# Kernel tuning notes

Hardware: AMD Instinct MI355X
Metric: run time of the kernel (lower is better)

## Reference

```python
import jax, jax.numpy as jnp
import numpy as np

N_NODES = 50000
N_EDGES = 800000
N_GRAPHS = 2500
HIDDEN = 64
IN_DIM = 14  # 11 QM9 features + 3 pos


def setup_inputs() -> dict:
    key = jax.random.key(0)
    ks = jax.random.split(key, 12)
    def glorot(k, shape):
        fan_in = shape[0]
        return jax.random.normal(k, shape, dtype=jnp.float32) / np.sqrt(fan_in)
    return {
        "x": jax.random.normal(ks[0], (N_NODES, 11), dtype=jnp.float32),
        "pos": jax.random.normal(ks[1], (N_NODES, 3), dtype=jnp.float32),
        "edge_index": jax.random.randint(ks[2], (2, N_EDGES), 0, N_NODES, dtype=jnp.int64),
        "batch": jnp.sort(jax.random.randint(ks[3], (N_NODES,), 0, N_GRAPHS, dtype=jnp.int64)),
        "W1a": glorot(ks[4], (IN_DIM, HIDDEN)),
        "b1a": jnp.zeros((HIDDEN,), jnp.float32),
        "W1b": glorot(ks[5], (HIDDEN, HIDDEN)),
        "b1b": jnp.zeros((HIDDEN,), jnp.float32),
        "W2a": glorot(ks[6], (HIDDEN, HIDDEN)),
        "b2a": jnp.zeros((HIDDEN,), jnp.float32),
        "W2b": glorot(ks[7], (HIDDEN, HIDDEN)),
        "b2b": jnp.zeros((HIDDEN,), jnp.float32),
        "Wlin": glorot(ks[8], (HIDDEN, 1)),
        "blin": jnp.zeros((1,), jnp.float32),
    }


def reference(x, pos, edge_index, batch, W1a, b1a, W1b, b1b, W2a, b2a, W2b, b2b, Wlin, blin):
    n = x.shape[0]
    src, dst = edge_index[0], edge_index[1]

    def gin_conv(h, Wa, ba, Wb, bb):
        # GINConv (eps=0): nn((1+eps)*h + sum_{j in N(i)} h_j)
        agg = jax.ops.segment_sum(h[src], dst, num_segments=n)  # scatter-add over edges
        z = h + agg
        return jax.nn.relu(z @ Wa + ba) @ Wb + bb

    h = jnp.concatenate([x, pos], axis=1)  # [N, 14]
    h = jax.nn.relu(gin_conv(h, W1a, b1a, W1b, b1b))
    h = jax.nn.relu(gin_conv(h, W2a, b2a, W2b, b2b))

    # global_mean_pool over graph ids
    sums = jax.ops.segment_sum(h, batch, num_segments=N_GRAPHS)            # [G, H]
    counts = jax.ops.segment_sum(jnp.ones((n,), h.dtype), batch, num_segments=N_GRAPHS)
    pooled = sums / jnp.maximum(counts, 1.0)[:, None]
    return pooled @ Wlin + blin  # [G, 1]
```

## Files before the change

### kernel.cpp

```cpp
#include <hip/hip_runtime.h>
#include <hip/hip_fp16.h>


typedef unsigned int uint;
typedef _Float16 half8 __attribute__((ext_vector_type(8)));
typedef float f32x4 __attribute__((ext_vector_type(4)));

#define BSH   6
#define NBKMAX 1024
#define EPB   4096
#define CAPSH 11
#define CAP   (1 << CAPSH)
#define ZBLK  64

__device__ __forceinline__ void addu(float* a, uint d) {
    __half2 h = *(__half2*)&d;
    a[0] += __low2float(h);
    a[1] += __high2float(h);
}
__device__ __forceinline__ half8 as_half8(uint4 u) {
    union { uint4 u; half8 h; } x; x.u = u; return x.h;
}


__global__ __launch_bounds__(256) void pack_bin(
    const float* __restrict__ x, const float* __restrict__ pos,
    uint2* __restrict__ xp2,
    const int* __restrict__ src, const int* __restrict__ dst,
    int* __restrict__ bkt_cnt, uint* __restrict__ pairs,
    const float* __restrict__ W1a, const float* __restrict__ W1b,
    const float* __restrict__ W2a, const float* __restrict__ W2b,
    _Float16* __restrict__ wp1a, _Float16* __restrict__ wp1b,
    _Float16* __restrict__ wp2a, _Float16* __restrict__ wp2b,
    uint4* __restrict__ zbuf, int nz4,
    int packb, int nbk, int N, int E)
{
    int bx = (int)blockIdx.x;
    if (bx < ZBLK) {
        uint4 z4 = {0u, 0u, 0u, 0u};
        for (int idx = bx * 256 + threadIdx.x; idx < nz4; idx += ZBLK * 256)
            zbuf[idx] = z4;
        return;
    }
    bx -= ZBLK;
    if (bx == 0) {
        for (int idx = threadIdx.x; idx < 64 * 32; idx += 256) {
            int n = idx >> 5, k = idx & 31;
            wp1a[idx] = (k < 14) ? (_Float16)W1a[k * 64 + n] : (_Float16)0.f;
        }
        for (int idx = threadIdx.x; idx < 64 * 64; idx += 256) {
            int n = idx >> 6, k = idx & 63;
            wp1b[idx] = (_Float16)W1b[k * 64 + n];
            wp2a[idx] = (_Float16)W2a[k * 64 + n];
            wp2b[idx] = (_Float16)W2b[k * 64 + n];
        }
        return;
    }
    bx -= 1;
    if (bx < packb) {
        int i = bx * 256 + threadIdx.x;
        if (i >= N) return;
        float v[16];
#pragma unroll
        for (int k = 0; k < 11; k++) v[k] = x[(size_t)i * 11 + k];
        v[11] = pos[(size_t)i * 3 + 0];
        v[12] = pos[(size_t)i * 3 + 1];
        v[13] = pos[(size_t)i * 3 + 2];
        v[14] = 0.f; v[15] = 0.f;
#pragma unroll
        for (int c = 0; c < 4; c++) {
            __half2 l = __floats2half2_rn(v[4 * c],     v[4 * c + 1]);
            __half2 h = __floats2half2_rn(v[4 * c + 2], v[4 * c + 3]);
            uint2 u;
            u.x = *(uint*)&l;
            u.y = *(uint*)&h;
            xp2[(size_t)i * 4 + c] = u;
        }
        return;
    }
    bx -= packb;
    __shared__ int lcnt[NBKMAX];
    __shared__ int lbase[NBKMAX];
    for (int i = threadIdx.x; i < nbk; i += 256) lcnt[i] = 0;
    __syncthreads();
    int e0 = bx * EPB + threadIdx.x;
    uint pv[EPB / 256];
    int  rk[EPB / 256], bk[EPB / 256];
#pragma unroll
    for (int j = 0; j < EPB / 256; j++) {
        int e = e0 + j * 256;
        bk[j] = -1;
        if (e < E) {
            int s = src[e];
            int d = dst[e];
            bk[j] = d >> BSH;
            pv[j] = ((uint)(d & ((1 << BSH) - 1)) << 16) | (uint)s;
            rk[j] = atomicAdd(&lcnt[bk[j]], 1);
        }
    }
    __syncthreads();
    for (int i = threadIdx.x; i < nbk; i += 256) {
        int c = lcnt[i];
        lbase[i] = c ? atomicAdd(&bkt_cnt[i], c) : 0;
    }
    __syncthreads();
#pragma unroll
    for (int j = 0; j < EPB / 256; j++) {
        if (bk[j] >= 0) {
            int p = lbase[bk[j]] + rk[j];
            if (p < CAP)
                pairs[((size_t)bk[j] << CAPSH) + p] = pv[j];
        }
    }
}


__global__ __launch_bounds__(256) void bucket_build(
    const uint* __restrict__ pairs, const int* __restrict__ bkt_cnt,
    int* __restrict__ offs, int* __restrict__ deg,
    int* __restrict__ ssrc, int N)
{
    __shared__ int cnt[256];
    __shared__ int cur[256];
    __shared__ int wsum[4];
    int b = blockIdx.x;
    int nbase = b << BSH;
    int nn = min(1 << BSH, N - nbase);
    cnt[threadIdx.x] = 0;
    __syncthreads();
    int start = b << CAPSH;
    int end = start + min(bkt_cnt[b], CAP);
    for (int e = start + threadIdx.x; e < end; e += 256)
        atomicAdd(&cnt[pairs[e] >> 16], 1);
    __syncthreads();
    int v = cnt[threadIdx.x];
    int lane = threadIdx.x & 63, w = threadIdx.x >> 6;
    int s = v;
#pragma unroll
    for (int off2 = 1; off2 < 64; off2 <<= 1) {
        int t = __shfl_up(s, off2, 64);
        if (lane >= off2) s += t;
    }
    if (lane == 63) wsum[w] = s;
    __syncthreads();
    int add = 0;
    for (int j = 0; j < w; j++) add += wsum[j];
    int gofs = start + (s + add - v);
    if (threadIdx.x < nn) {
        offs[nbase + threadIdx.x] = gofs;
        deg[nbase + threadIdx.x]  = v;
    }
    cur[threadIdx.x] = gofs;
    __syncthreads();
    for (int e = start + threadIdx.x; e < end; e += 256) {
        uint pr = pairs[e];
        int p = atomicAdd(&cur[pr >> 16], 1);
        ssrc[p] = (int)(pr & 0xffffu);
    }
}


__global__ __launch_bounds__(256) void gather1_mlp1(
    const uint2* __restrict__ xp2,
    const int* __restrict__ offs, const int* __restrict__ deg,
    const int* __restrict__ ssrc,
    const _Float16* __restrict__ wp1a, const _Float16* __restrict__ wp1b,
    const float* __restrict__ b1a, const float* __restrict__ b1b,
    uint* __restrict__ h1p)
{
    __shared__ uint4 zb[16 * 2];
    __shared__ float hb[16 * 68];
    int lane = threadIdx.x & 63;
    int wid  = threadIdx.x >> 6;
    int i0 = blockIdx.x << 4;
    int n0 = i0 + wid * 4;

    int stv = 0, lnv = 0;
    if (lane < 4) { stv = offs[n0 + lane]; lnv = deg[n0 + lane]; }
    int j4 = lane >> 2, c = lane & 3;
    int svp[4];
#pragma unroll
    for (int t = 0; t < 4; t++) {
        int st = __shfl(stv, t, 64), len = __shfl(lnv, t, 64);
        if (len > 0) svp[t] = ssrc[st + min(lane, len - 1)];
    }
    for (int t = 0; t < 4; t++) {
        int i = n0 + t;
        int st = __shfl(stv, t, 64), len = __shfl(lnv, t, 64);
        uint2 S = xp2[(size_t)i * 4 + c];
        float a[4] = {0.f, 0.f, 0.f, 0.f};
        int k = 0;
        while (k < len) {
            int chunk = min(len - k, 64);
            int sv = (k == 0) ? svp[t]
                              : ssrc[st + k + min(lane, chunk - 1)];
            int tt = 0;
            for (; tt + 32 <= chunk; tt += 32) {
                int sA = __shfl(sv, tt + j4, 64);
                int sB = __shfl(sv, tt + 16 + j4, 64);
                uint2 A = xp2[(size_t)sA * 4 + c];
                uint2 B = xp2[(size_t)sB * 4 + c];
                addu(a + 0, A.x); addu(a + 2, A.y);
                addu(a + 0, B.x); addu(a + 2, B.y);
            }
            for (; tt + 16 <= chunk; tt += 16) {
                int sA = __shfl(sv, tt + j4, 64);
                uint2 A = xp2[(size_t)sA * 4 + c];
                addu(a + 0, A.x); addu(a + 2, A.y);
            }
            if (tt < chunk) {
                int r = chunk - tt;
                int sA = __shfl(sv, tt + min(j4, r - 1), 64);
                uint2 A = xp2[(size_t)sA * 4 + c];
                if (j4 < r) { addu(a + 0, A.x); addu(a + 2, A.y); }
            }
            k += chunk;
        }
#pragma unroll
        for (int mm = 4; mm < 64; mm <<= 1)
#pragma unroll
            for (int d = 0; d < 4; d++) a[d] += __shfl_xor(a[d], mm, 64);
        addu(a + 0, S.x); addu(a + 2, S.y);
        if (lane < 4) {
            __half2 l  = __floats2half2_rn(a[0], a[1]);
            __half2 hh = __floats2half2_rn(a[2], a[3]);
            uint2 u;
            u.x = *(uint*)&l;
            u.y = *(uint*)&hh;
            ((uint2*)zb)[(wid * 4 + t) * 4 + lane] = u;
        }
    }
    __syncthreads();

    int m = lane & 15, quad = lane >> 4;
    int half = lane >> 5, p = lane & 31;
    int nw = wid * 16 + m;
    half8 BA  = *(const half8*)(wp1a + (size_t)nw * 32 + quad * 8);
    half8 BB0 = *(const half8*)(wp1b + (size_t)nw * 64 + quad * 8);
    half8 BB1 = *(const half8*)(wp1b + (size_t)nw * 64 + 32 + quad * 8);
    float baw = b1a[nw], bbw = b1b[nw];

    half8 A0;
#pragma unroll
    for (int jj = 0; jj < 8; jj++) A0[jj] = (_Float16)0.f;
    if (quad < 2)
        A0 = as_half8(zb[m * 2 + quad]);
    f32x4 acc = (f32x4){baw, baw, baw, baw};
    acc = __builtin_amdgcn_mfma_f32_16x16x32_f16(A0, BA, acc, 0, 0, 0);
#pragma unroll
    for (int r = 0; r < 4; r++)
        hb[(quad * 4 + r) * 68 + wid * 16 + m] = fmaxf(acc[r], 0.f);
    __syncthreads();
    half8 A1[2];
#pragma unroll
    for (int hh = 0; hh < 2; hh++)
#pragma unroll
        for (int jj = 0; jj < 8; jj++)
            A1[hh][jj] = (_Float16)hb[m * 68 + hh * 32 + quad * 8 + jj];
    f32x4 acc2 = (f32x4){bbw, bbw, bbw, bbw};
    acc2 = __builtin_amdgcn_mfma_f32_16x16x32_f16(A1[0], BB0, acc2, 0, 0, 0);
    acc2 = __builtin_amdgcn_mfma_f32_16x16x32_f16(A1[1], BB1, acc2, 0, 0, 0);
    __syncthreads();
#pragma unroll
    for (int r = 0; r < 4; r++)
        hb[(quad * 4 + r) * 68 + wid * 16 + m] = fmaxf(acc2[r], 0.f);
    __syncthreads();
#pragma unroll
    for (int it = 0; it < 2; it++) {
        int row = wid * 4 + it * 2 + half;
        float lo = hb[row * 68 + 2 * p];
        float hi = hb[row * 68 + 2 * p + 1];
        __half2 hh2 = __floats2half2_rn(lo, hi);
        h1p[(size_t)(i0 + row) * 32 + p] = *(uint*)&hh2;
    }
}


__global__ __launch_bounds__(256) void gather2_mlp2pool(
    const uint4* __restrict__ h4,
    const int* __restrict__ offs, const int* __restrict__ deg,
    const int* __restrict__ ssrc,
    const _Float16* __restrict__ wp2a, const _Float16* __restrict__ wp2b,
    const float* __restrict__ b2a, const float* __restrict__ b2b,
    const int* __restrict__ batch,
    float* __restrict__ sums, float* __restrict__ counts)
{
    __shared__ uint4 zb[16 * 8];
    __shared__ float hb[16 * 68];
    int lane = threadIdx.x & 63;
    int wid  = threadIdx.x >> 6;
    int i0 = blockIdx.x << 4;
    int n0 = i0 + wid * 4;

    int stv = 0, lnv = 0;
    if (lane < 4) { stv = offs[n0 + lane]; lnv = deg[n0 + lane]; }
    int j8 = lane >> 3, q = lane & 7;
    int svp[4];
#pragma unroll
    for (int t = 0; t < 4; t++) {
        int st = __shfl(stv, t, 64), len = __shfl(lnv, t, 64);
        if (len > 0) svp[t] = ssrc[st + min(lane, len - 1)];
    }
    for (int t = 0; t < 4; t++) {
        int i = n0 + t;
        int st = __shfl(stv, t, 64), len = __shfl(lnv, t, 64);
        uint4 S = h4[(size_t)i * 8 + q];
        float a[8] = {0.f, 0.f, 0.f, 0.f, 0.f, 0.f, 0.f, 0.f};
        int k = 0;
        while (k < len) {
            int chunk = min(len - k, 64);
            int sv = (k == 0) ? svp[t]
                              : ssrc[st + k + min(lane, chunk - 1)];
            int tt = 0;
            for (; tt + 32 <= chunk; tt += 32) {
                int sA = __shfl(sv, tt + j8, 64);
                int sB = __shfl(sv, tt + 8 + j8, 64);
                int sC = __shfl(sv, tt + 16 + j8, 64);
                int sD = __shfl(sv, tt + 24 + j8, 64);
                uint4 A = h4[(size_t)sA * 8 + q];
                uint4 B = h4[(size_t)sB * 8 + q];
                uint4 C = h4[(size_t)sC * 8 + q];
                uint4 D = h4[(size_t)sD * 8 + q];
                addu(a + 0, A.x); addu(a + 2, A.y); addu(a + 4, A.z); addu(a + 6, A.w);
                addu(a + 0, B.x); addu(a + 2, B.y); addu(a + 4, B.z); addu(a + 6, B.w);
                addu(a + 0, C.x); addu(a + 2, C.y); addu(a + 4, C.z); addu(a + 6, C.w);
                addu(a + 0, D.x); addu(a + 2, D.y); addu(a + 4, D.z); addu(a + 6, D.w);
            }
            for (; tt + 16 <= chunk; tt += 16) {
                int sA = __shfl(sv, tt + j8, 64);
                int sB = __shfl(sv, tt + 8 + j8, 64);
                uint4 A = h4[(size_t)sA * 8 + q];
                uint4 B = h4[(size_t)sB * 8 + q];
                addu(a + 0, A.x); addu(a + 2, A.y); addu(a + 4, A.z); addu(a + 6, A.w);
                addu(a + 0, B.x); addu(a + 2, B.y); addu(a + 4, B.z); addu(a + 6, B.w);
            }
            for (; tt + 8 <= chunk; tt += 8) {
                int sA = __shfl(sv, tt + j8, 64);
                uint4 A = h4[(size_t)sA * 8 + q];
                addu(a + 0, A.x); addu(a + 2, A.y); addu(a + 4, A.z); addu(a + 6, A.w);
            }
            if (tt < chunk) {
                int r = chunk - tt;
                int sA = __shfl(sv, tt + min(j8, r - 1), 64);
                uint4 A = h4[(size_t)sA * 8 + q];
                if (j8 < r) {
                    addu(a + 0, A.x); addu(a + 2, A.y);
                    addu(a + 4, A.z); addu(a + 6, A.w);
                }
            }
            k += chunk;
        }
#pragma unroll
        for (int mm = 8; mm < 64; mm <<= 1)
#pragma unroll
            for (int d = 0; d < 8; d++) a[d] += __shfl_xor(a[d], mm, 64);
        addu(a + 0, S.x); addu(a + 2, S.y); addu(a + 4, S.z); addu(a + 6, S.w);
        if (lane < 8) {
            __half2 p0 = __floats2half2_rn(a[0], a[1]);
            __half2 p1 = __floats2half2_rn(a[2], a[3]);
            __half2 p2 = __floats2half2_rn(a[4], a[5]);
            __half2 p3 = __floats2half2_rn(a[6], a[7]);
            uint4 o4;
            o4.x = *(uint*)&p0; o4.y = *(uint*)&p1;
            o4.z = *(uint*)&p2; o4.w = *(uint*)&p3;
            zb[(wid * 4 + t) * 8 + lane] = o4;
        }
    }
    __syncthreads();

    int m = lane & 15, quad = lane >> 4;
    int nw = wid * 16 + m;
    half8 BA0 = *(const half8*)(wp2a + (size_t)nw * 64 + quad * 8);
    half8 BA1 = *(const half8*)(wp2a + (size_t)nw * 64 + 32 + quad * 8);
    half8 BB0 = *(const half8*)(wp2b + (size_t)nw * 64 + quad * 8);
    half8 BB1 = *(const half8*)(wp2b + (size_t)nw * 64 + 32 + quad * 8);
    float baw = b2a[nw], bbw = b2b[nw];

    half8 A0[2];
#pragma unroll
    for (int hh = 0; hh < 2; hh++)
        A0[hh] = as_half8(zb[m * 8 + hh * 4 + quad]);
    f32x4 acc = (f32x4){baw, baw, baw, baw};
    acc = __builtin_amdgcn_mfma_f32_16x16x32_f16(A0[0], BA0, acc, 0, 0, 0);
    acc = __builtin_amdgcn_mfma_f32_16x16x32_f16(A0[1], BA1, acc, 0, 0, 0);
#pragma unroll
    for (int r = 0; r < 4; r++)
        hb[(quad * 4 + r) * 68 + wid * 16 + m] = fmaxf(acc[r], 0.f);
    __syncthreads();
    half8 A1[2];
#pragma unroll
    for (int hh = 0; hh < 2; hh++)
#pragma unroll
        for (int jj = 0; jj < 8; jj++)
            A1[hh][jj] = (_Float16)hb[m * 68 + hh * 32 + quad * 8 + jj];
    f32x4 acc2 = (f32x4){bbw, bbw, bbw, bbw};
    acc2 = __builtin_amdgcn_mfma_f32_16x16x32_f16(A1[0], BB0, acc2, 0, 0, 0);
    acc2 = __builtin_amdgcn_mfma_f32_16x16x32_f16(A1[1], BB1, acc2, 0, 0, 0);
    __syncthreads();
#pragma unroll
    for (int r = 0; r < 4; r++)
        hb[(quad * 4 + r) * 68 + wid * 16 + m] = fmaxf(acc2[r], 0.f);
    __syncthreads();

    int gcur = batch[i0 + wid * 4]; float ps = 0.f; int cntn = 0;
#pragma unroll
    for (int nn = 0; nn < 4; nn++) {
        int row = wid * 4 + nn;
        float v = hb[row * 68 + lane];
        int gi = batch[i0 + row];
        if (gi != gcur) {
            atomicAdd(&sums[gcur * 64 + lane], ps);
            if (lane == 0) atomicAdd(&counts[gcur], (float)cntn);
            gcur = gi; ps = 0.f; cntn = 0;
        }
        ps += v; cntn++;
    }
    atomicAdd(&sums[gcur * 64 + lane], ps);
    if (lane == 0) atomicAdd(&counts[gcur], (float)cntn);
}

__global__ __launch_bounds__(256) void gin_final(
    const float* __restrict__ sums, const float* __restrict__ counts,
    const float* __restrict__ Wlin, const float* __restrict__ blin,
    float* __restrict__ out, int G)
{
    int lane = threadIdx.x & 63;
    int g    = blockIdx.x * 4 + (threadIdx.x >> 6);
    if (g < G) {
        float v = sums[g * 64 + lane] * Wlin[lane];
#pragma unroll
        for (int off = 32; off > 0; off >>= 1) v += __shfl_down(v, off, 64);
        if (lane == 0) out[g] = v / fmaxf(counts[g], 1.0f) + blin[0];
    }
}

extern "C" void kernel_launch(void* const* d_in, const int* in_sizes, int n_in,
                              void* d_out, int out_size, void* d_ws, size_t ws_size,
                              hipStream_t stream) {
    const float* x    = (const float*)d_in[0];
    const float* pos  = (const float*)d_in[1];
    const int*   ei   = (const int*)d_in[2];
    const int*   batch= (const int*)d_in[3];
    const float* W1a  = (const float*)d_in[4];
    const float* b1a  = (const float*)d_in[5];
    const float* W1b  = (const float*)d_in[6];
    const float* b1b  = (const float*)d_in[7];
    const float* W2a  = (const float*)d_in[8];
    const float* b2a  = (const float*)d_in[9];
    const float* W2b  = (const float*)d_in[10];
    const float* b2b  = (const float*)d_in[11];
    const float* Wlin = (const float*)d_in[12];
    const float* blin = (const float*)d_in[13];
    float* out = (float*)d_out;

    const int N = in_sizes[0] / 11;
    const int E = in_sizes[2] / 2;
    const int G = out_size;

    const int* src = ei;
    const int* dst = ei + E;
    const int nbk   = (N + (1 << BSH) - 1) >> BSH;
    const int packb = (N + 255) / 256;
    const int neb   = (E + EPB - 1) / EPB;
    const int NG    = N >> 4;

    char* ws = (char*)d_ws;
    size_t o = 0;
    float* sums    = (float*)(ws + o); o += (size_t)G * 64 * 4;
    float* counts  = (float*)(ws + o); o += (((size_t)G + 63) & ~(size_t)63) * 4;
    const int nz4  = (int)(((size_t)G * 64 + (((size_t)G + 63) & ~(size_t)63)) / 4);
    int*   bkt_cnt = (int*)(ws + o);   o += NBKMAX * 4;
    o = (o + 255) & ~(size_t)255;
    _Float16* wp1a = (_Float16*)(ws + o); o += 64 * 32 * 2;
    o = (o + 255) & ~(size_t)255;
    _Float16* wp1b = (_Float16*)(ws + o); o += 64 * 64 * 2;
    o = (o + 255) & ~(size_t)255;
    _Float16* wp2a = (_Float16*)(ws + o); o += 64 * 64 * 2;
    o = (o + 255) & ~(size_t)255;
    _Float16* wp2b = (_Float16*)(ws + o); o += 64 * 64 * 2;
    o = (o + 255) & ~(size_t)255;
    int*   offs    = (int*)(ws + o);   o += (size_t)N * 4;
    int*   deg     = (int*)(ws + o);   o += (size_t)N * 4;
    o = (o + 255) & ~(size_t)255;
    int*   ssrc    = (int*)(ws + o);   o += ((size_t)nbk << CAPSH) * 4;
    o = (o + 255) & ~(size_t)255;
    uint*  h1p     = (uint*)(ws + o);  o += (size_t)N * 32 * 4;
    o = (o + 255) & ~(size_t)255;
    uint2* xp2     = (uint2*)(ws + o); o += (size_t)N * 32;
    o = (o + 255) & ~(size_t)255;
    uint*  pairs   = (uint*)(ws + o);  o += ((size_t)nbk << CAPSH) * 4;

    hipMemsetAsync(bkt_cnt, 0, NBKMAX * 4, stream);

    pack_bin<<<ZBLK + 1 + packb + neb, 256, 0, stream>>>(
        x, pos, xp2, src, dst, bkt_cnt, pairs,
        W1a, W1b, W2a, W2b, wp1a, wp1b, wp2a, wp2b,
        (uint4*)sums, nz4, packb, nbk, N, E);
    bucket_build<<<nbk, 256, 0, stream>>>(pairs, bkt_cnt, offs, deg, ssrc, N);
    gather1_mlp1<<<NG, 256, 0, stream>>>(
        xp2, offs, deg, ssrc, wp1a, wp1b, b1a, b1b, h1p);
    gather2_mlp2pool<<<NG, 256, 0, stream>>>(
        (const uint4*)h1p, offs, deg, ssrc, wp2a, wp2b, b2a, b2b,
        batch, sums, counts);
    gin_final<<<(G + 3) / 4, 256, 0, stream>>>(
        sums, counts, Wlin, blin, out, G);
}
```

Baseline: 160.9 us.

## Replace bucketed CSR build with direct atomic scatter into fixed-capacity neighbor slots

Drops the two-pass bucket binning plus the bucket_build kernel. Each edge now takes a slot with a global atomicAdd on its destination's degree and writes its source into a padded per-node neighbor array of 64 entries. The gather kernels then read a node's neighbors from a fixed offset, with no offsets array and no chunk loop. This removes one kernel launch and an intermediate pass over the edges. In exchange it adds 800k global atomics, scattered 4-byte writes into a 12.8MB array, and silently drops any edges beyond 64 per node. Neighbor order is also no longer deterministic.

Result: slower. 195.9 us (+21.8%).

```diff
diff --git a/kernel.cpp b/kernel.cpp
--- a/kernel.cpp
+++ b/kernel.cpp
@@ -6,12 +6,9 @@
 typedef _Float16 half8 __attribute__((ext_vector_type(8)));
 typedef float f32x4 __attribute__((ext_vector_type(4)));
 
-#define BSH   6
-#define NBKMAX 1024
-#define EPB   4096
-#define CAPSH 11
-#define CAP   (1 << CAPSH)
-#define ZBLK  64
+#define EPB   1024
+#define ZBLK  32
+#define CAPN  64
 
 __device__ __forceinline__ void addu(float* a, uint d) {
     __half2 h = *(__half2*)&d;
@@ -23,17 +20,17 @@
 }
 
 
-__global__ __launch_bounds__(256) void pack_bin(
+__global__ __launch_bounds__(256) void pack_scatter(
     const float* __restrict__ x, const float* __restrict__ pos,
     uint2* __restrict__ xp2,
     const int* __restrict__ src, const int* __restrict__ dst,
-    int* __restrict__ bkt_cnt, uint* __restrict__ pairs,
+    int* __restrict__ deg, int* __restrict__ nbr,
     const float* __restrict__ W1a, const float* __restrict__ W1b,
     const float* __restrict__ W2a, const float* __restrict__ W2b,
     _Float16* __restrict__ wp1a, _Float16* __restrict__ wp1b,
     _Float16* __restrict__ wp2a, _Float16* __restrict__ wp2b,
     uint4* __restrict__ zbuf, int nz4,
-    int packb, int nbk, int N, int E)
+    int packb, int N, int E)
 {
     int bx = (int)blockIdx.x;
     if (bx < ZBLK) {
@@ -79,91 +76,24 @@
         return;
     }
     bx -= packb;
-    __shared__ int lcnt[NBKMAX];
-    __shared__ int lbase[NBKMAX];
-    for (int i = threadIdx.x; i < nbk; i += 256) lcnt[i] = 0;
-    __syncthreads();
     int e0 = bx * EPB + threadIdx.x;
-    uint pv[EPB / 256];
-    int  rk[EPB / 256], bk[EPB / 256];
 #pragma unroll
     for (int j = 0; j < EPB / 256; j++) {
         int e = e0 + j * 256;
-        bk[j] = -1;
         if (e < E) {
             int s = src[e];
             int d = dst[e];
-            bk[j] = d >> BSH;
-            pv[j] = ((uint)(d & ((1 << BSH) - 1)) << 16) | (uint)s;
-            rk[j] = atomicAdd(&lcnt[bk[j]], 1);
-        }
-    }
-    __syncthreads();
-    for (int i = threadIdx.x; i < nbk; i += 256) {
-        int c = lcnt[i];
-        lbase[i] = c ? atomicAdd(&bkt_cnt[i], c) : 0;
-    }
-    __syncthreads();
-#pragma unroll
-    for (int j = 0; j < EPB / 256; j++) {
-        if (bk[j] >= 0) {
-            int p = lbase[bk[j]] + rk[j];
-            if (p < CAP)
-                pairs[((size_t)bk[j] << CAPSH) + p] = pv[j];
-        }
-    }
-}
-
-
-__global__ __launch_bounds__(256) void bucket_build(
-    const uint* __restrict__ pairs, const int* __restrict__ bkt_cnt,
-    int* __restrict__ offs, int* __restrict__ deg,
-    int* __restrict__ ssrc, int N)
-{
-    __shared__ int cnt[256];
-    __shared__ int cur[256];
-    __shared__ int wsum[4];
-    int b = blockIdx.x;
-    int nbase = b << BSH;
-    int nn = min(1 << BSH, N - nbase);
-    cnt[threadIdx.x] = 0;
-    __syncthreads();
-    int start = b << CAPSH;
-    int end = start + min(bkt_cnt[b], CAP);
-    for (int e = start + threadIdx.x; e < end; e += 256)
-        atomicAdd(&cnt[pairs[e] >> 16], 1);
-    __syncthreads();
-    int v = cnt[threadIdx.x];
-    int lane = threadIdx.x & 63, w = threadIdx.x >> 6;
-    int s = v;
-#pragma unroll
-    for (int off2 = 1; off2 < 64; off2 <<= 1) {
-        int t = __shfl_up(s, off2, 64);
-        if (lane >= off2) s += t;
-    }
-    if (lane == 63) wsum[w] = s;
-    __syncthreads();
-    int add = 0;
-    for (int j = 0; j < w; j++) add += wsum[j];
-    int gofs = start + (s + add - v);
-    if (threadIdx.x < nn) {
-        offs[nbase + threadIdx.x] = gofs;
-        deg[nbase + threadIdx.x]  = v;
-    }
-    cur[threadIdx.x] = gofs;
-    __syncthreads();
-    for (int e = start + threadIdx.x; e < end; e += 256) {
-        uint pr = pairs[e];
-        int p = atomicAdd(&cur[pr >> 16], 1);
-        ssrc[p] = (int)(pr & 0xffffu);
+            int r = atomicAdd(&deg[d], 1);
+            if (r < CAPN)
+                nbr[((size_t)d << 6) + r] = s;
+        }
     }
 }
 
 
 __global__ __launch_bounds__(256) void gather1_mlp1(
     const uint2* __restrict__ xp2,
-    const int* __restrict__ offs, const int* __restrict__ deg,
-    const int* __restrict__ ssrc,
+    const int* __restrict__ deg, const int* __restrict__ nbr,
     const _Float16* __restrict__ wp1a, const _Float16* __restrict__ wp1b,
     const float* __restrict__ b1a, const float* __restrict__ b1b,
     uint* __restrict__ h1p)
@@ -175,46 +105,40 @@
     int i0 = blockIdx.x << 4;
     int n0 = i0 + wid * 4;
 
-    int stv = 0, lnv = 0;
-    if (lane < 4) { stv = offs[n0 + lane]; lnv = deg[n0 + lane]; }
+    int lnv = 0;
+    if (lane < 4) lnv = min(deg[n0 + lane], CAPN);
     int j4 = lane >> 2, c = lane & 3;
     int svp[4];
 #pragma unroll
     for (int t = 0; t < 4; t++) {
-        int st = __shfl(stv, t, 64), len = __shfl(lnv, t, 64);
-        if (len > 0) svp[t] = ssrc[st + min(lane, len - 1)];
+        int len = __shfl(lnv, t, 64);
+        if (len > 0) svp[t] = nbr[((size_t)(n0 + t) << 6) + min(lane, len - 1)];
     }
     for (int t = 0; t < 4; t++) {
         int i = n0 + t;
-        int st = __shfl(stv, t, 64), len = __shfl(lnv, t, 64);
+        int len = __shfl(lnv, t, 64);
         uint2 S = xp2[(size_t)i * 4 + c];
         float a[4] = {0.f, 0.f, 0.f, 0.f};
-        int k = 0;
-        while (k < len) {
-            int chunk = min(len - k, 64);
-            int sv = (k == 0) ? svp[t]
-                              : ssrc[st + k + min(lane, chunk - 1)];
-            int tt = 0;
-            for (; tt + 32 <= chunk; tt += 32) {
-                int sA = __shfl(sv, tt + j4, 64);
-                int sB = __shfl(sv, tt + 16 + j4, 64);
-                uint2 A = xp2[(size_t)sA * 4 + c];
-                uint2 B = xp2[(size_t)sB * 4 + c];
-                addu(a + 0, A.x); addu(a + 2, A.y);
-                addu(a + 0, B.x); addu(a + 2, B.y);
-            }
-            for (; tt + 16 <= chunk; tt += 16) {
-                int sA = __shfl(sv, tt + j4, 64);
-                uint2 A = xp2[(size_t)sA * 4 + c];
-                addu(a + 0, A.x); addu(a + 2, A.y);
-            }
-            if (tt < chunk) {
-                int r = chunk - tt;
-                int sA = __shfl(sv, tt + min(j4, r - 1), 64);
-                uint2 A = xp2[(size_t)sA * 4 + c];
-                if (j4 < r) { addu(a + 0, A.x); addu(a + 2, A.y); }
-            }
-            k += chunk;
+        int sv = svp[t];
+        int tt = 0;
+        for (; tt + 32 <= len; tt += 32) {
+            int sA = __shfl(sv, tt + j4, 64);
+            int sB = __shfl(sv, tt + 16 + j4, 64);
+            uint2 A = xp2[(size_t)sA * 4 + c];
+            uint2 B = xp2[(size_t)sB * 4 + c];
+            addu(a + 0, A.x); addu(a + 2, A.y);
+            addu(a + 0, B.x); addu(a + 2, B.y);
+        }
+        for (; tt + 16 <= len; tt += 16) {
+            int sA = __shfl(sv, tt + j4, 64);
+            uint2 A = xp2[(size_t)sA * 4 + c];
+            addu(a + 0, A.x); addu(a + 2, A.y);
+        }
+        if (tt < len) {
+            int r = len - tt;
+            int sA = __shfl(sv, tt + min(j4, r - 1), 64);
+            uint2 A = xp2[(size_t)sA * 4 + c];
+            if (j4 < r) { addu(a + 0, A.x); addu(a + 2, A.y); }
         }
 #pragma unroll
         for (int mm = 4; mm < 64; mm <<= 1)
@@ -278,8 +202,7 @@
 
 __global__ __launch_bounds__(256) void gather2_mlp2pool(
     const uint4* __restrict__ h4,
-    const int* __restrict__ offs, const int* __restrict__ deg,
-    const int* __restrict__ ssrc,
+    const int* __restrict__ deg, const int* __restrict__ nbr,
     const _Float16* __restrict__ wp2a, const _Float16* __restrict__ wp2b,
     const float* __restrict__ b2a, const float* __restrict__ b2b,
     const int* __restrict__ batch,
@@ -292,63 +215,57 @@
     int i0 = blockIdx.x << 4;
     int n0 = i0 + wid * 4;
 
-    int stv = 0, lnv = 0;
-    if (lane < 4) { stv = offs[n0 + lane]; lnv = deg[n0 + lane]; }
+    int lnv = 0;
+    if (lane < 4) lnv = min(deg[n0 + lane], CAPN);
     int j8 = lane >> 3, q = lane & 7;
     int svp[4];
 #pragma unroll
     for (int t = 0; t < 4; t++) {
-        int st = __shfl(stv, t, 64), len = __shfl(lnv, t, 64);
-        if (len > 0) svp[t] = ssrc[st + min(lane, len - 1)];
+        int len = __shfl(lnv, t, 64);
+        if (len > 0) svp[t] = nbr[((size_t)(n0 + t) << 6) + min(lane, len - 1)];
     }
     for (int t = 0; t < 4; t++) {
         int i = n0 + t;
-        int st = __shfl(stv, t, 64), len = __shfl(lnv, t, 64);
+        int len = __shfl(lnv, t, 64);
         uint4 S = h4[(size_t)i * 8 + q];
         float a[8] = {0.f, 0.f, 0.f, 0.f, 0.f, 0.f, 0.f, 0.f};
-        int k = 0;
-        while (k < len) {
-            int chunk = min(len - k, 64);
-            int sv = (k == 0) ? svp[t]
-                              : ssrc[st + k + min(lane, chunk - 1)];
-            int tt = 0;
-            for (; tt + 32 <= chunk; tt += 32) {
-                int sA = __shfl(sv, tt + j8, 64);
-                int sB = __shfl(sv, tt + 8 + j8, 64);
-                int sC = __shfl(sv, tt + 16 + j8, 64);
-                int sD = __shfl(sv, tt + 24 + j8, 64);
-                uint4 A = h4[(size_t)sA * 8 + q];
-                uint4 B = h4[(size_t)sB * 8 + q];
-                uint4 C = h4[(size_t)sC * 8 + q];
-                uint4 D = h4[(size_t)sD * 8 + q];
-                addu(a + 0, A.x); addu(a + 2, A.y); addu(a + 4, A.z); addu(a + 6, A.w);
-                addu(a + 0, B.x); addu(a + 2, B.y); addu(a + 4, B.z); addu(a + 6, B.w);
-                addu(a + 0, C.x); addu(a + 2, C.y); addu(a + 4, C.z); addu(a + 6, C.w);
-                addu(a + 0, D.x); addu(a + 2, D.y); addu(a + 4, D.z); addu(a + 6, D.w);
+        int sv = svp[t];
+        int tt = 0;
+        for (; tt + 32 <= len; tt += 32) {
+            int sA = __shfl(sv, tt + j8, 64);
+            int sB = __shfl(sv, tt + 8 + j8, 64);
+            int sC = __shfl(sv, tt + 16 + j8, 64);
+            int sD = __shfl(sv, tt + 24 + j8, 64);
+            uint4 A = h4[(size_t)sA * 8 + q];
+            uint4 B = h4[(size_t)sB * 8 + q];
+            uint4 C = h4[(size_t)sC * 8 + q];
+            uint4 D = h4[(size_t)sD * 8 + q];
+            addu(a + 0, A.x); addu(a + 2, A.y); addu(a + 4, A.z); addu(a + 6, A.w);
+            addu(a + 0, B.x); addu(a + 2, B.y); addu(a + 4, B.z); addu(a + 6, B.w);
+            addu(a + 0, C.x); addu(a + 2, C.y); addu(a + 4, C.z); addu(a + 6, C.w);
+            addu(a + 0, D.x); addu(a + 2, D.y); addu(a + 4, D.z); addu(a + 6, D.w);
+        }
+        for (; tt + 16 <= len; tt += 16) {
+            int sA = __shfl(sv, tt + j8, 64);
+            int sB = __shfl(sv, tt + 8 + j8, 64);
+            uint4 A = h4[(size_t)sA * 8 + q];
+            uint4 B = h4[(size_t)sB * 8 + q];
+            addu(a + 0, A.x); addu(a + 2, A.y); addu(a + 4, A.z); addu(a + 6, A.w);
+            addu(a + 0, B.x); addu(a + 2, B.y); addu(a + 4, B.z); addu(a + 6, B.w);
+        }
+        for (; tt + 8 <= len; tt += 8) {
+            int sA = __shfl(sv, tt + j8, 64);
+            uint4 A = h4[(size_t)sA * 8 + q];
+            addu(a + 0, A.x); addu(a + 2, A.y); addu(a + 4, A.z); addu(a + 6, A.w);
+        }
+        if (tt < len) {
+            int r = len - tt;
+            int sA = __shfl(sv, tt + min(j8, r - 1), 64);
+            uint4 A = h4[(size_t)sA * 8 + q];
+            if (j8 < r) {
+                addu(a + 0, A.x); addu(a + 2, A.y);
+                addu(a + 4, A.z); addu(a + 6, A.w);
             }
-            for (; tt + 16 <= chunk; tt += 16) {
-                int sA = __shfl(sv, tt + j8, 64);
-                int sB = __shfl(sv, tt + 8 + j8, 64);
-                uint4 A = h4[(size_t)sA * 8 + q];
-                uint4 B = h4[(size_t)sB * 8 + q];
-                addu(a + 0, A.x); addu(a + 2, A.y); addu(a + 4, A.z); addu(a + 6, A.w);
-                addu(a + 0, B.x); addu(a + 2, B.y); addu(a + 4, B.z); addu(a + 6, B.w);
-            }
-            for (; tt + 8 <= chunk; tt += 8) {
-                int sA = __shfl(sv, tt + j8, 64);
-                uint4 A = h4[(size_t)sA * 8 + q];
-                addu(a + 0, A.x); addu(a + 2, A.y); addu(a + 4, A.z); addu(a + 6, A.w);
-            }
-            if (tt < chunk) {
-                int r = chunk - tt;
-                int sA = __shfl(sv, tt + min(j8, r - 1), 64);
-                uint4 A = h4[(size_t)sA * 8 + q];
-                if (j8 < r) {
-                    addu(a + 0, A.x); addu(a + 2, A.y);
-                    addu(a + 4, A.z); addu(a + 6, A.w);
-                }
-            }
-            k += chunk;
         }
 #pragma unroll
         for (int mm = 8; mm < 64; mm <<= 1)
@@ -459,7 +376,6 @@
 
     const int* src = ei;
     const int* dst = ei + E;
-    const int nbk   = (N + (1 << BSH) - 1) >> BSH;
     const int packb = (N + 255) / 256;
     const int neb   = (E + EPB - 1) / EPB;
     const int NG    = N >> 4;
@@ -469,7 +385,7 @@
     float* sums    = (float*)(ws + o); o += (size_t)G * 64 * 4;
     float* counts  = (float*)(ws + o); o += (((size_t)G + 63) & ~(size_t)63) * 4;
     const int nz4  = (int)(((size_t)G * 64 + (((size_t)G + 63) & ~(size_t)63)) / 4);
-    int*   bkt_cnt = (int*)(ws + o);   o += NBKMAX * 4;
+    int*   deg     = (int*)(ws + o);   o += (size_t)N * 4;
     o = (o + 255) & ~(size_t)255;
     _Float16* wp1a = (_Float16*)(ws + o); o += 64 * 32 * 2;
     o = (o + 255) & ~(size_t)255;
@@ -479,28 +395,22 @@
     o = (o + 255) & ~(size_t)255;
     _Float16* wp2b = (_Float16*)(ws + o); o += 64 * 64 * 2;
     o = (o + 255) & ~(size_t)255;
-    int*   offs    = (int*)(ws + o);   o += (size_t)N * 4;
-    int*   deg     = (int*)(ws + o);   o += (size_t)N * 4;
-    o = (o + 255) & ~(size_t)255;
-    int*   ssrc    = (int*)(ws + o);   o += ((size_t)nbk << CAPSH) * 4;
+    int*   nbr     = (int*)(ws + o);   o += (size_t)N * CAPN * 4;
     o = (o + 255) & ~(size_t)255;
     uint*  h1p     = (uint*)(ws + o);  o += (size_t)N * 32 * 4;
     o = (o + 255) & ~(size_t)255;
     uint2* xp2     = (uint2*)(ws + o); o += (size_t)N * 32;
-    o = (o + 255) & ~(size_t)255;
-    uint*  pairs   = (uint*)(ws + o);  o += ((size_t)nbk << CAPSH) * 4;
-
-    hipMemsetAsync(bkt_cnt, 0, NBKMAX * 4, stream);
-
-    pack_bin<<<ZBLK + 1 + packb + neb, 256, 0, stream>>>(
-        x, pos, xp2, src, dst, bkt_cnt, pairs,
+
+    hipMemsetAsync(deg, 0, (size_t)N * 4, stream);
+
+    pack_scatter<<<ZBLK + 1 + packb + neb, 256, 0, stream>>>(
+        x, pos, xp2, src, dst, deg, nbr,
         W1a, W1b, W2a, W2b, wp1a, wp1b, wp2a, wp2b,
-        (uint4*)sums, nz4, packb, nbk, N, E);
-    bucket_build<<<nbk, 256, 0, stream>>>(pairs, bkt_cnt, offs, deg, ssrc, N);
+        (uint4*)sums, nz4, packb, N, E);
     gather1_mlp1<<<NG, 256, 0, stream>>>(
-        xp2, offs, deg, ssrc, wp1a, wp1b, b1a, b1b, h1p);
+        xp2, deg, nbr, wp1a, wp1b, b1a, b1b, h1p);
     gather2_mlp2pool<<<NG, 256, 0, stream>>>(
-        (const uint4*)h1p, offs, deg, ssrc, wp2a, wp2b, b2a, b2b,
+        (const uint4*)h1p, deg, nbr, wp2a, wp2b, b2a, b2b,
         batch, sums, counts);
     gin_final<<<(G + 3) / 4, 256, 0, stream>>>(
         sums, counts, Wlin, blin, out, G);
```

## Gather neighbors of four nodes concurrently per wavefront with 16-lane groups

Applied to the files above, without the earlier changes.

Rewrites the neighbor-aggregation phase of both fused gather+MLP kernels. Each wave previously walked its four nodes one after another with all 64 lanes. It now gives each node a 16-lane group that covers the first 32 neighbors through preloaded indices in unrolled loads, plus a tail loop for higher degrees. With average degree around 16, most lanes in the old layout idled on masked work and serialized per-node reductions. The new layout cuts the shuffle reduction depth and overlaps loads across nodes, but it adds divergence when degrees are uneven.

After: 147.8 us. 8.1% less time.

```diff
diff --git a/kernel.cpp b/kernel.cpp
--- a/kernel.cpp
+++ b/kernel.cpp
@@ -177,58 +177,60 @@
 
     int stv = 0, lnv = 0;
     if (lane < 4) { stv = offs[n0 + lane]; lnv = deg[n0 + lane]; }
-    int j4 = lane >> 2, c = lane & 3;
-    int svp[4];
-#pragma unroll
-    for (int t = 0; t < 4; t++) {
-        int st = __shfl(stv, t, 64), len = __shfl(lnv, t, 64);
-        if (len > 0) svp[t] = ssrc[st + min(lane, len - 1)];
-    }
-    for (int t = 0; t < 4; t++) {
-        int i = n0 + t;
-        int st = __shfl(stv, t, 64), len = __shfl(lnv, t, 64);
-        uint2 S = xp2[(size_t)i * 4 + c];
-        float a[4] = {0.f, 0.f, 0.f, 0.f};
-        int k = 0;
-        while (k < len) {
-            int chunk = min(len - k, 64);
-            int sv = (k == 0) ? svp[t]
-                              : ssrc[st + k + min(lane, chunk - 1)];
-            int tt = 0;
-            for (; tt + 32 <= chunk; tt += 32) {
-                int sA = __shfl(sv, tt + j4, 64);
-                int sB = __shfl(sv, tt + 16 + j4, 64);
-                uint2 A = xp2[(size_t)sA * 4 + c];
-                uint2 B = xp2[(size_t)sB * 4 + c];
-                addu(a + 0, A.x); addu(a + 2, A.y);
-                addu(a + 0, B.x); addu(a + 2, B.y);
-            }
-            for (; tt + 16 <= chunk; tt += 16) {
-                int sA = __shfl(sv, tt + j4, 64);
-                uint2 A = xp2[(size_t)sA * 4 + c];
+    int n  = lane >> 4;
+    int s  = (lane >> 2) & 3;
+    int c  = lane & 3;
+    int dn = __shfl(lnv, n, 64);
+    int st = __shfl(stv, n, 64);
+    int pA = lane & 15;
+    int svA = 0, svB = 0;
+    if (dn > 0)  svA = ssrc[st + min(pA, dn - 1)];
+    if (dn > 16) svB = ssrc[st + min(16 + pA, dn - 1)];
+    uint2 S = {0u, 0u};
+    if (s == 0) S = xp2[(size_t)(n0 + n) * 4 + c];
+
+    float a[4] = {0.f, 0.f, 0.f, 0.f};
+#pragma unroll
+    for (int it = 0; it < 4; ++it) {
+        int pos = it * 4 + s;
+        int sA = __shfl(svA, (n << 4) | pos, 64);
+        if (pos < dn) {
+            uint2 A = xp2[(size_t)sA * 4 + c];
+            addu(a + 0, A.x); addu(a + 2, A.y);
+        }
+    }
+    if (__any(dn > 16)) {
+#pragma unroll
+        for (int it = 4; it < 8; ++it) {
+            int pos = it * 4 + s;
+            int sB = __shfl(svB, (n << 4) | (pos - 16), 64);
+            if (pos < dn) {
+                uint2 A = xp2[(size_t)sB * 4 + c];
                 addu(a + 0, A.x); addu(a + 2, A.y);
             }
-            if (tt < chunk) {
-                int r = chunk - tt;
-                int sA = __shfl(sv, tt + min(j4, r - 1), 64);
-                uint2 A = xp2[(size_t)sA * 4 + c];
-                if (j4 < r) { addu(a + 0, A.x); addu(a + 2, A.y); }
+        }
+        int pos2 = 32 + s;
+        while (__any(pos2 < dn)) {
+            if (pos2 < dn) {
+                int sid = ssrc[st + pos2];
+                uint2 A = xp2[(size_t)sid * 4 + c];
+                addu(a + 0, A.x); addu(a + 2, A.y);
             }
-            k += chunk;
-        }
-#pragma unroll
-        for (int mm = 4; mm < 64; mm <<= 1)
-#pragma unroll
-            for (int d = 0; d < 4; d++) a[d] += __shfl_xor(a[d], mm, 64);
+            pos2 += 4;
+        }
+    }
+#pragma unroll
+    for (int mm = 4; mm <= 8; mm <<= 1)
+#pragma unroll
+        for (int d = 0; d < 4; d++) a[d] += __shfl_xor(a[d], mm, 64);
+    if (s == 0) {
         addu(a + 0, S.x); addu(a + 2, S.y);
-        if (lane < 4) {
-            __half2 l  = __floats2half2_rn(a[0], a[1]);
-            __half2 hh = __floats2half2_rn(a[2], a[3]);
-            uint2 u;
-            u.x = *(uint*)&l;
-            u.y = *(uint*)&hh;
-            ((uint2*)zb)[(wid * 4 + t) * 4 + lane] = u;
-        }
+        __half2 l  = __floats2half2_rn(a[0], a[1]);
+        __half2 hh = __floats2half2_rn(a[2], a[3]);
+        uint2 u;
+        u.x = *(uint*)&l;
+        u.y = *(uint*)&hh;
+        ((uint2*)zb)[(wid * 4 + n) * 4 + c] = u;
     }
     __syncthreads();
 
@@ -294,77 +296,60 @@
 
     int stv = 0, lnv = 0;
     if (lane < 4) { stv = offs[n0 + lane]; lnv = deg[n0 + lane]; }
-    int j8 = lane >> 3, q = lane & 7;
-    int svp[4];
-#pragma unroll
-    for (int t = 0; t < 4; t++) {
-        int st = __shfl(stv, t, 64), len = __shfl(lnv, t, 64);
-        if (len > 0) svp[t] = ssrc[st + min(lane, len - 1)];
-    }
-    for (int t = 0; t < 4; t++) {
-        int i = n0 + t;
-        int st = __shfl(stv, t, 64), len = __shfl(lnv, t, 64);
-        uint4 S = h4[(size_t)i * 8 + q];
-        float a[8] = {0.f, 0.f, 0.f, 0.f, 0.f, 0.f, 0.f, 0.f};
-        int k = 0;
-        while (k < len) {
-            int chunk = min(len - k, 64);
-            int sv = (k == 0) ? svp[t]
-                              : ssrc[st + k + min(lane, chunk - 1)];
-            int tt = 0;
-            for (; tt + 32 <= chunk; tt += 32) {
-                int sA = __shfl(sv, tt + j8, 64);
-                int sB = __shfl(sv, tt + 8 + j8, 64);
-                int sC = __shfl(sv, tt + 16 + j8, 64);
-                int sD = __shfl(sv, tt + 24 + j8, 64);
-                uint4 A = h4[(size_t)sA * 8 + q];
-                uint4 B = h4[(size_t)sB * 8 + q];
-                uint4 C = h4[(size_t)sC * 8 + q];
-                uint4 D = h4[(size_t)sD * 8 + q];
-                addu(a + 0, A.x); addu(a + 2, A.y); addu(a + 4, A.z); addu(a + 6, A.w);
-                addu(a + 0, B.x); addu(a + 2, B.y); addu(a + 4, B.z); addu(a + 6, B.w);
-                addu(a + 0, C.x); addu(a + 2, C.y); addu(a + 4, C.z); addu(a + 6, C.w);
-                addu(a + 0, D.x); addu(a + 2, D.y); addu(a + 4, D.z); addu(a + 6, D.w);
-            }
-            for (; tt + 16 <= chunk; tt += 16) {
-                int sA = __shfl(sv, tt + j8, 64);
-                int sB = __shfl(sv, tt + 8 + j8, 64);
-                uint4 A = h4[(size_t)sA * 8 + q];
-                uint4 B = h4[(size_t)sB * 8 + q];
-                addu(a + 0, A.x); addu(a + 2, A.y); addu(a + 4, A.z); addu(a + 6, A.w);
-                addu(a + 0, B.x); addu(a + 2, B.y); addu(a + 4, B.z); addu(a + 6, B.w);
-            }
-            for (; tt + 8 <= chunk; tt += 8) {
-                int sA = __shfl(sv, tt + j8, 64);
-                uint4 A = h4[(size_t)sA * 8 + q];
+    int n  = lane >> 4;
+    int s  = (lane >> 3) & 1;
+    int q  = lane & 7;
+    int dn = __shfl(lnv, n, 64);
+    int st = __shfl(stv, n, 64);
+    int pA = lane & 15;
+    int svA = 0, svB = 0;
+    if (dn > 0)  svA = ssrc[st + min(pA, dn - 1)];
+    if (dn > 16) svB = ssrc[st + min(16 + pA, dn - 1)];
+    uint4 S = {0u, 0u, 0u, 0u};
+    if (s == 0) S = h4[(size_t)(n0 + n) * 8 + q];
+
+    float a[8] = {0.f, 0.f, 0.f, 0.f, 0.f, 0.f, 0.f, 0.f};
+#pragma unroll
+    for (int it = 0; it < 8; ++it) {
+        int pos = it * 2 + s;
+        int sA = __shfl(svA, (n << 4) | pos, 64);
+        if (pos < dn) {
+            uint4 A = h4[(size_t)sA * 8 + q];
+            addu(a + 0, A.x); addu(a + 2, A.y); addu(a + 4, A.z); addu(a + 6, A.w);
+        }
+    }
+    if (__any(dn > 16)) {
+#pragma unroll
+        for (int it = 8; it < 16; ++it) {
+            int pos = it * 2 + s;
+            int sB = __shfl(svB, (n << 4) | (pos - 16), 64);
+            if (pos < dn) {
+                uint4 A = h4[(size_t)sB * 8 + q];
                 addu(a + 0, A.x); addu(a + 2, A.y); addu(a + 4, A.z); addu(a + 6, A.w);
             }
-            if (tt < chunk) {
-                int r = chunk - tt;
-                int sA = __shfl(sv, tt + min(j8, r - 1), 64);
-                uint4 A = h4[(size_t)sA * 8 + q];
-                if (j8 < r) {
-                    addu(a + 0, A.x); addu(a + 2, A.y);
-                    addu(a + 4, A.z); addu(a + 6, A.w);
-                }
+        }
+        int pos2 = 32 + s;
+        while (__any(pos2 < dn)) {
+            if (pos2 < dn) {
+                int sid = ssrc[st + pos2];
+                uint4 A = h4[(size_t)sid * 8 + q];
+                addu(a + 0, A.x); addu(a + 2, A.y); addu(a + 4, A.z); addu(a + 6, A.w);
             }
-            k += chunk;
-        }
-#pragma unroll
-        for (int mm = 8; mm < 64; mm <<= 1)
-#pragma unroll
-            for (int d = 0; d < 8; d++) a[d] += __shfl_xor(a[d], mm, 64);
+            pos2 += 2;
+        }
+    }
+#pragma unroll
+    for (int d = 0; d < 8; d++) a[d] += __shfl_xor(a[d], 8, 64);
+    if (s == 0) {
         addu(a + 0, S.x); addu(a + 2, S.y); addu(a + 4, S.z); addu(a + 6, S.w);
-        if (lane < 8) {
-            __half2 p0 = __floats2half2_rn(a[0], a[1]);
-            __half2 p1 = __floats2half2_rn(a[2], a[3]);
-            __half2 p2 = __floats2half2_rn(a[4], a[5]);
-            __half2 p3 = __floats2half2_rn(a[6], a[7]);
-            uint4 o4;
-            o4.x = *(uint*)&p0; o4.y = *(uint*)&p1;
-            o4.z = *(uint*)&p2; o4.w = *(uint*)&p3;
-            zb[(wid * 4 + t) * 8 + lane] = o4;
-        }
+        __half2 p0 = __floats2half2_rn(a[0], a[1]);
+        __half2 p1 = __floats2half2_rn(a[2], a[3]);
+        __half2 p2 = __floats2half2_rn(a[4], a[5]);
+        __half2 p3 = __floats2half2_rn(a[6], a[7]);
+        uint4 o4;
+        o4.x = *(uint*)&p0; o4.y = *(uint*)&p1;
+        o4.z = *(uint*)&p2; o4.w = *(uint*)&p3;
+        zb[(wid * 4 + n) * 8 + q] = o4;
     }
     __syncthreads();
 
```
